# Performance work log

Hardware: AMD Instinct MI355X
Metric: run time of the kernel (lower is better)

Reference implementation:

```python
import jax, jax.numpy as jnp
import numpy as np

B = 32        # num graphs
N = 512       # nodes per graph (equal-sized blocks)
HID = 512     # hidden_dim
H = 8         # num_heads
E = 262144    # num edges
ED = 16       # edge feature dim


def setup_inputs() -> dict:
    key = jax.random.key(0)
    ks = jax.random.split(key, 12)
    x = jax.random.normal(ks[0], (B * N, HID), jnp.float32)
    # contiguous, sorted graph assignment (equal-sized graphs)
    batch = jnp.repeat(jnp.arange(B, dtype=jnp.int64), N)
    # within-graph random edges
    g = jax.random.randint(ks[1], (E,), 0, B)
    src = g * N + jax.random.randint(ks[2], (E,), 0, N)
    dst = g * N + jax.random.randint(ks[3], (E,), 0, N)
    edge_index = jnp.stack([src, dst]).astype(jnp.int64)
    edge_attr = jax.random.normal(ks[4], (E, ED), jnp.float32)
    s = 1.0 / np.sqrt(HID).astype(np.float32)
    Wq = jax.random.normal(ks[5], (HID, HID), jnp.float32) * s
    Wk = jax.random.normal(ks[6], (HID, HID), jnp.float32) * s
    Wv = jax.random.normal(ks[7], (HID, HID), jnp.float32) * s
    Wo = jax.random.normal(ks[8], (HID, HID), jnp.float32) * s
    We = jax.random.normal(ks[9], (ED, H), jnp.float32) * (1.0 / np.sqrt(ED).astype(np.float32))
    bq = jnp.zeros((HID,), jnp.float32)
    bk = jnp.zeros((HID,), jnp.float32)
    bv = jnp.zeros((HID,), jnp.float32)
    bo = jnp.zeros((HID,), jnp.float32)
    be = jnp.zeros((H,), jnp.float32)
    return dict(x=x, batch=batch, edge_index=edge_index, edge_attr=edge_attr,
                Wq=Wq, bq=bq, Wk=Wk, bk=bk, Wv=Wv, bv=bv, Wo=Wo, bo=bo,
                We=We, be=be, num_graphs=B)


def reference(x, batch, edge_index, edge_attr, Wq, bq, Wk, bk, Wv, bv, Wo, bo, We, be, num_graphs):
    n_total, hid = x.shape
    n = n_total // num_graphs           # nodes per graph (equal blocks)
    hd = hid // H                       # head_dim
    scale = 1.0 / jnp.sqrt(jnp.asarray(hd, x.dtype))
    q = (x @ Wq + bq).reshape(num_graphs, n, H, hd)
    k = (x @ Wk + bk).reshape(num_graphs, n, H, hd)
    v = (x @ Wv + bv).reshape(num_graphs, n, H, hd)
    # per-graph dense scores: [B, n(query), m(key), H]
    attn = jnp.einsum('bnhd,bmhd->bnmh', q, k) * scale
    # edge-bias scatter-add (edges are intra-graph; local coords via div/mod)
    eb = edge_attr @ We + be                      # [E, H]
    b_idx = edge_index[0] // n
    loc_src = edge_index[0] % n
    loc_dst = edge_index[1] % n
    attn = attn.at[b_idx, loc_src, loc_dst].add(eb)
    # softmax over key axis (torch dim=1 of 'nmh' == axis 2 here)
    attn = jax.nn.softmax(attn, axis=2)
    out = jnp.einsum('bnmh,bmhd->bnhd', attn, v).reshape(n_total, hid)
    return out @ Wo + bo
```

## Files before the change

### kernel.cpp

```cpp
#include <hip/hip_runtime.h>
#include <stdint.h>

typedef unsigned short u16;
typedef __bf16 bf16x8 __attribute__((ext_vector_type(8)));
typedef short  short8 __attribute__((ext_vector_type(8)));
typedef float  f32x4  __attribute__((ext_vector_type(4)));
typedef float  float4v __attribute__((ext_vector_type(4)));
typedef uint32_t u32x2 __attribute__((ext_vector_type(2)));

#define NG    32
#define NPG   512
#define HIDD  512
#define NH    8
#define HD    64
#define NE    262144
#define NNODE (NG*NPG)

__device__ __forceinline__ float fexp2(float x) { return __builtin_amdgcn_exp2f(x); }

__device__ __forceinline__ u16 f2bf(float f) {
  union { float f; uint32_t u; } x; x.f = f;
  uint32_t r = x.u + 0x7FFFu + ((x.u >> 16) & 1u);
  return (u16)(r >> 16);
}
__device__ __forceinline__ float bf2f(u16 b) {
  union { uint32_t u; float f; } x; x.u = ((uint32_t)b) << 16;
  return x.f;
}
__device__ __forceinline__ uint32_t pkbf(float a, float b) {
  __bf16 x = (__bf16)a, y = (__bf16)b;
  return (uint32_t)__builtin_bit_cast(u16, x) | ((uint32_t)__builtin_bit_cast(u16, y) << 16);
}
__device__ __forceinline__ bf16x8 ldfrag(const u16* p) {
  short8 t = *(const short8*)p;
  return __builtin_bit_cast(bf16x8, t);
}
__device__ __forceinline__ f32x4 mfma16(bf16x8 a, bf16x8 b, f32x4 c) {
  return __builtin_amdgcn_mfma_f32_16x16x32_bf16(a, b, c, 0, 0, 0);
}
__device__ __forceinline__ void gl2lds16(const void* g, void* l) {
  __builtin_amdgcn_global_load_lds((const __attribute__((address_space(1))) void*)g,
                                   (__attribute__((address_space(3))) void*)l, 16, 0, 0);
}
__device__ __forceinline__ void st(u16* p, float v)   { *p = f2bf(v); }
__device__ __forceinline__ void st(float* p, float v) { *p = v; }


__global__ void k_cast_x(const float* __restrict__ x, u16* __restrict__ xb) {
  size_t i = ((size_t)blockIdx.x * 256 + threadIdx.x) * 8;
  float4v v0 = *(const float4v*)(x + i);
  float4v v1 = *(const float4v*)(x + i + 4);
  short8 r;
  r[0]=(short)f2bf(v0[0]); r[1]=(short)f2bf(v0[1]); r[2]=(short)f2bf(v0[2]); r[3]=(short)f2bf(v0[3]);
  r[4]=(short)f2bf(v1[0]); r[5]=(short)f2bf(v1[1]); r[6]=(short)f2bf(v1[2]); r[7]=(short)f2bf(v1[3]);
  *(short8*)(xb + i) = r;
}

__global__ void k_transw(const float* __restrict__ W0, const float* __restrict__ W1,
                         const float* __restrict__ W2, const float* __restrict__ W3,
                         u16* __restrict__ wt) {
  const float* W = blockIdx.z==0 ? W0 : blockIdx.z==1 ? W1 : blockIdx.z==2 ? W2 : W3;
  u16* out = wt + (size_t)blockIdx.z * HIDD * HIDD;
  __shared__ float tl[32][33];
  int tx = threadIdx.x, ty = threadIdx.y;
  int x0 = blockIdx.x * 32, y0 = blockIdx.y * 32;
  #pragma unroll
  for (int i = 0; i < 4; ++i) tl[ty + i*8][tx] = W[(size_t)(y0 + ty + i*8) * HIDD + x0 + tx];
  __syncthreads();
  #pragma unroll
  for (int i = 0; i < 4; ++i) out[(size_t)(x0 + ty + i*8) * HIDD + (y0 + tx)] = f2bf(tl[tx][ty + i*8]);
}

__global__ void k_count2(const int* __restrict__ ei, int* __restrict__ counts) {
  int e = blockIdx.x * 256 + threadIdx.x;
  int src = ei[e];
  int dl  = ei[NE + e] & (NPG - 1);
  atomicAdd(&counts[src * 8 + (dl >> 6)], 1);
}

__global__ void k_scan_a(const int* __restrict__ counts, int* __restrict__ rowstart,
                         int* __restrict__ bsum) {
  __shared__ int arr[256];
  int t = threadIdx.x;
  int i = blockIdx.x * 256 + t;
  int c = counts[i];
  arr[t] = c;
  __syncthreads();
  for (int off = 1; off < 256; off <<= 1) {
    int v = (t >= off) ? arr[t - off] : 0;
    __syncthreads();
    arr[t] += v;
    __syncthreads();
  }
  rowstart[i] = arr[t] - c;
  if (t == 255) bsum[blockIdx.x] = arr[255];
}
__global__ void k_scan_b(int* __restrict__ bsum) {
  __shared__ int arr[512];
  int t = threadIdx.x;
  int c = bsum[t];
  arr[t] = c;
  __syncthreads();
  for (int off = 1; off < 512; off <<= 1) {
    int v = (t >= off) ? arr[t - off] : 0;
    __syncthreads();
    arr[t] += v;
    __syncthreads();
  }
  bsum[t] = arr[t] - c;
}
__global__ void k_scan_c(const int* __restrict__ bsum, int* __restrict__ rowstart) {
  int i = blockIdx.x * 256 + threadIdx.x;
  rowstart[i] += bsum[blockIdx.x];
  if (i == 0) rowstart[131072] = NE;
}

__global__ void k_fill(const int* __restrict__ ei, const float* __restrict__ ea,
                       const float* __restrict__ We, const float* __restrict__ be,
                       const int* __restrict__ rowstart, int* __restrict__ cursor,
                       uint32_t* __restrict__ packed) {
  __shared__ float w[128];
  __shared__ float bb[8];
  int t = threadIdx.x;
  if (t < 128) w[t] = We[t];
  if (t < 8)   bb[t] = be[t];
  __syncthreads();
  int e = blockIdx.x * 256 + t;
  int src = ei[e];
  int dl  = ei[NE + e] & (NPG - 1);
  const float* ap = ea + (size_t)e * 16;
  float a[16];
  #pragma unroll
  for (int i = 0; i < 16; i += 4) {
    float4v v = *(const float4v*)(ap + i);
    a[i]=v[0]; a[i+1]=v[1]; a[i+2]=v[2]; a[i+3]=v[3];
  }
  float acc[8];
  #pragma unroll
  for (int hh = 0; hh < 8; ++hh) acc[hh] = bb[hh];
  #pragma unroll
  for (int d = 0; d < 16; ++d)
    #pragma unroll
    for (int hh = 0; hh < 8; ++hh) acc[hh] += a[d] * w[d*8 + hh];
  int bin = src * 8 + (dl >> 6);
  int pos = atomicAdd(&cursor[bin], 1);
  size_t base = ((size_t)(rowstart[bin] + pos)) * 8;
  #pragma unroll
  for (int hh = 0; hh < 8; ++hh) {
    float m = fexp2(acc[hh] * 1.44269504089f);
    union { _Float16 hf; u16 us; } cv; cv.hf = (_Float16)m;
    packed[base + hh] = (uint32_t)(dl & 63) | ((uint32_t)cv.us << 16);
  }
}


template <typename OT, bool VOUT>
__device__ void gemm_body(u16* smem, const u16* __restrict__ A, const u16* __restrict__ Bt,
                          const float* __restrict__ bias, OT* __restrict__ C,
                          u16* __restrict__ vtg) {
  const int tid = threadIdx.x;
  const int w = tid >> 6, l = tid & 63, lr = l & 15, lg = l >> 4;
  const int bm0 = blockIdx.y * 128, bn0 = blockIdx.x * 128;
  const int wr = w >> 1, wc = w & 1;
  f32x4 acc[4][4];
  #pragma unroll
  for (int i = 0; i < 4; ++i)
    #pragma unroll
    for (int j = 0; j < 4; ++j) acc[i][j] = (f32x4){0.f, 0.f, 0.f, 0.f};

  const int o1 = w * 1024 + l * 16;
  auto stageAB = [&](int kt, int buf) {
    #pragma unroll
    for (int rnd = 0; rnd < 2; ++rnd) {
      const int o = rnd * 4096 + o1;
      const int row = o >> 6, colb = o & 63;
      gl2lds16((const char*)A  + ((size_t)(bm0 + row) * HIDD + kt * 32) * 2 + colb,
               (char*)smem + buf * 8192 + o);
      gl2lds16((const char*)Bt + ((size_t)(bn0 + row) * HIDD + kt * 32) * 2 + colb,
               (char*)smem + 16384 + buf * 8192 + o);
    }
  };

  stageAB(0, 0);
  for (int kt = 0; kt < 16; ++kt) {
    if (kt < 15) {
      stageAB(kt + 1, (kt + 1) & 1);
      asm volatile("s_waitcnt vmcnt(4)" ::: "memory");
    } else {
      asm volatile("s_waitcnt vmcnt(0)" ::: "memory");
    }
    __syncthreads();
    const u16* Ab = smem + (kt & 1) * 4096;
    const u16* Bb = smem + 8192 + (kt & 1) * 4096;
    bf16x8 af[4], bfr[4];
    #pragma unroll
    for (int i = 0; i < 4; ++i) af[i]  = ldfrag(&Ab[(wr*64 + i*16 + lr) * 32 + lg*8]);
    #pragma unroll
    for (int j = 0; j < 4; ++j) bfr[j] = ldfrag(&Bb[(wc*64 + j*16 + lr) * 32 + lg*8]);
    #pragma unroll
    for (int i = 0; i < 4; ++i)
      #pragma unroll
      for (int j = 0; j < 4; ++j)
        acc[i][j] = mfma16(af[i], bfr[j], acc[i][j]);
    __syncthreads();
  }

  if constexpr (VOUT) {
    #pragma unroll
    for (int j = 0; j < 4; ++j) {
      const int d = j * 16 + lr;
      const float bv = bias[bn0 + wc*64 + j*16 + lr];
      #pragma unroll
      for (int i = 0; i < 4; ++i) {
        const int t4 = wc * 2 + wr;
        const int byteo = t4 * 8192 + d * 128 + ((i*32 + lg*8) ^ ((d & 7) << 4));
        uint32_t lo = pkbf(acc[i][j][0] + bv, acc[i][j][1] + bv);
        uint32_t hi = pkbf(acc[i][j][2] + bv, acc[i][j][3] + bv);
        *(u32x2*)((char*)smem + byteo) = (u32x2){lo, hi};
      }
    }
    __syncthreads();
    const int b = bm0 >> 9, kt0 = (bm0 & 511) >> 6, h0 = bn0 >> 6;
    #pragma unroll
    for (int t4 = 0; t4 < 4; ++t4) {
      size_t base = ((size_t)(b * 8 + h0 + (t4 >> 1)) * 8 + kt0 + (t4 & 1)) * 4096;
      #pragma unroll
      for (int rnd = 0; rnd < 2; ++rnd) {
        int idx = rnd * 256 + tid;
        *(short8*)(vtg + base + idx * 8) = *(const short8*)&smem[t4 * 4096 + idx * 8];
      }
    }
  } else {
    #pragma unroll
    for (int j = 0; j < 4; ++j) {
      const int col = bn0 + wc*64 + j*16 + lr;
      const float bv = bias[col];
      #pragma unroll
      for (int i = 0; i < 4; ++i) {
        const int row0 = bm0 + wr*64 + i*16 + lg*4;
        #pragma unroll
        for (int q = 0; q < 4; ++q)
          st(&C[(size_t)(row0 + q) * HIDD + col], acc[i][j][q] + bv);
      }
    }
  }
}

__global__ __launch_bounds__(256, 3) void k_gemm_qkv(
    const u16* __restrict__ A, const u16* __restrict__ Wt,
    const float* __restrict__ b0, const float* __restrict__ b1, const float* __restrict__ b2,
    u16* __restrict__ O0, u16* __restrict__ O1, u16* __restrict__ vtg) {
  __shared__ u16 smem[16384];
  int z = blockIdx.z;
  const u16* Bt = Wt + (size_t)z * HIDD * HIDD;
  if (z == 0)      gemm_body<u16, false>(smem, A, Bt, b0, O0, nullptr);
  else if (z == 1) gemm_body<u16, false>(smem, A, Bt, b1, O1, nullptr);
  else             gemm_body<u16, true >(smem, A, Bt, b2, nullptr, vtg);
}

__global__ __launch_bounds__(256, 3) void k_gemm_out(
    const u16* __restrict__ A, const u16* __restrict__ Bt,
    const float* __restrict__ bias, float* __restrict__ C) {
  __shared__ u16 smem[16384];
  gemm_body<float, false>(smem, A, Bt, bias, C, nullptr);
}


__global__ __launch_bounds__(256, 4) void k_attn(
    const u16* __restrict__ qb, const u16* __restrict__ kb, const u16* __restrict__ vtg,
    const uint32_t* __restrict__ packed, const int* __restrict__ rowstart2,
    u16* __restrict__ ab) {
  __shared__ u16 kl[2][4096];
  __shared__ u16 vl[2][4096];
  __shared__ u16 pl[4][1024];
  const int tid = threadIdx.x, w = tid >> 6, l = tid & 63, lr = l & 15, lg = l >> 4;

  const int id = blockIdx.x;
  const int nid = (id & 7) * 256 + (id >> 3);
  const int q0 = (nid & 7) * 64;
  const int h  = (nid >> 3) & 7;
  const int b  = nid >> 6;
  const int bh = b * 8 + h;
  const int row = w * 16 + lr;
  const int grow = b * NPG + q0 + row;
  u16* plw = &pl[w][0];
  const int pswz = (lr & 7) << 4;

  bf16x8 qf[2];
  {
    const u16* qp = qb + (size_t)grow * HIDD + h * HD + lg * 8;
    qf[0] = ldfrag(qp);
    qf[1] = ldfrag(qp + 32);
  }

  auto stageK = [&](int kt, int buf) {
    #pragma unroll
    for (int rnd = 0; rnd < 2; ++rnd) {
      int o = rnd * 4096 + w * 1024 + l * 16;
      int key = o >> 7, db = o & 127;
      int col = db ^ ((key & 7) << 4);
      gl2lds16((const char*)kb + ((size_t)(b * NPG + kt * 64 + key) * HIDD + h * HD) * 2 + col,
               (char*)kl + buf * 8192 + o);
    }
  };
  auto stageV = [&](int kt, int buf) {
    #pragma unroll
    for (int rnd = 0; rnd < 2; ++rnd) {
      int o = rnd * 4096 + w * 1024 + l * 16;
      gl2lds16((const char*)vtg + ((size_t)(bh * 8 + kt)) * 8192 + o,
               (char*)vl + buf * 8192 + o);
    }
  };

  const float c1 = 0.125f * 1.44269504089f;
  float m2 = -1e30f;
  float rowsum = 0.f;
  f32x4 oacc[4];
  #pragma unroll
  for (int dt = 0; dt < 4; ++dt) oacc[dt] = (f32x4){0.f, 0.f, 0.f, 0.f};

  stageK(0, 0); stageV(0, 0); stageK(1, 1); stageV(1, 1);

  int eA = rowstart2[grow * 8];
  int eB = rowstart2[grow * 8 + 1];

  for (int kt = 0; kt < 8; ++kt) {
    int eC = (kt < 7) ? rowstart2[grow * 8 + kt + 2] : 0;
    if (kt < 7) asm volatile("s_waitcnt vmcnt(4)" ::: "memory");
    else        asm volatile("s_waitcnt vmcnt(0)" ::: "memory");
    __syncthreads();

    const u16* kB = kl[kt & 1];
    f32x4 s4[4];
    __builtin_amdgcn_s_setprio(1);
    #pragma unroll
    for (int sub = 0; sub < 4; ++sub) {
      s4[sub] = (f32x4){0.f, 0.f, 0.f, 0.f};
      int key = sub * 16 + lr;
      #pragma unroll
      for (int ks = 0; ks < 2; ++ks) {
        int db = ((ks * 32 + lg * 8) * 2) ^ ((key & 7) << 4);
        bf16x8 kf = ldfrag(&kB[(key * 128 + db) >> 1]);
        s4[sub] = mfma16(kf, qf[ks], s4[sub]);
      }
    }
    __builtin_amdgcn_s_setprio(0);

    float tm = s4[0][0];
    #pragma unroll
    for (int sub = 0; sub < 4; ++sub)
      #pragma unroll
      for (int e = 0; e < 4; ++e) tm = fmaxf(tm, s4[sub][e]);
    tm = fmaxf(tm, __shfl_xor(tm, 16, 64));
    tm = fmaxf(tm, __shfl_xor(tm, 32, 64));
    float tmc = tm * c1;
    if (__any(tmc > m2 + 8.0f)) {
      float m2n = fmaxf(m2, tmc);
      float rsc = fexp2(m2 - m2n);
      m2 = m2n;
      rowsum *= rsc;
      #pragma unroll
      for (int dt = 0; dt < 4; ++dt) oacc[dt] *= rsc;
    }

    #pragma unroll
    for (int sub = 0; sub < 4; ++sub) {
      float p0 = fexp2(__builtin_fmaf(s4[sub][0], c1, -m2));
      float p1 = fexp2(__builtin_fmaf(s4[sub][1], c1, -m2));
      float p2 = fexp2(__builtin_fmaf(s4[sub][2], c1, -m2));
      float p3 = fexp2(__builtin_fmaf(s4[sub][3], c1, -m2));
      rowsum += (p0 + p1) + (p2 + p3);
      uint32_t lo = pkbf(p0, p1);
      uint32_t hi = pkbf(p2, p3);
      *(u32x2*)((char*)plw + lr * 128 + ((sub * 32 + lg * 8) ^ pswz)) = (u32x2){lo, hi};
    }
    asm volatile("s_waitcnt lgkmcnt(0)" ::: "memory");
    __builtin_amdgcn_sched_barrier(0);

    {
      float delta = 0.f;
      for (int s = eA; s < eB; ++s) {
        uint32_t u = packed[(size_t)s * 8 + h];
        int dl = (int)(u & 63u);
        if ((dl & 3) == lg) {
          union { u16 us; _Float16 hf; } cv; cv.us = (u16)(u >> 16);
          float mult = (float)cv.hf;
          int idx = (lr * 128 + ((dl * 2) ^ pswz)) >> 1;
          float old = bf2f(plw[idx]);
          u16 nb = f2bf(old * mult);
          plw[idx] = nb;
          delta += bf2f(nb) - old;
        }
      }
      rowsum += delta;
    }
    asm volatile("s_waitcnt lgkmcnt(0)" ::: "memory");
    __builtin_amdgcn_sched_barrier(0);

    const u16* vB = vl[kt & 1];
    __builtin_amdgcn_s_setprio(1);
    #pragma unroll
    for (int ks = 0; ks < 2; ++ks) {
      bf16x8 pa = ldfrag(&plw[(lr * 128 + ((ks * 64 + lg * 16) ^ pswz)) >> 1]);
      #pragma unroll
      for (int dt = 0; dt < 4; ++dt) {
        int d = dt * 16 + lr;
        bf16x8 vf = ldfrag(&vB[(d * 128 + ((ks * 64 + lg * 16) ^ ((d & 7) << 4))) >> 1]);
        oacc[dt] = mfma16(vf, pa, oacc[dt]);
      }
    }
    __builtin_amdgcn_s_setprio(0);

    __syncthreads();
    if (kt < 6) { stageK(kt + 2, kt & 1); stageV(kt + 2, kt & 1); }
    eA = eB; eB = eC;
  }

  float tot = rowsum + __shfl_xor(rowsum, 16, 64);
  tot += __shfl_xor(tot, 32, 64);
  float inv = 1.0f / tot;
  #pragma unroll
  for (int dt = 0; dt < 4; ++dt) {
    uint32_t lo = pkbf(oacc[dt][0] * inv, oacc[dt][1] * inv);
    uint32_t hi = pkbf(oacc[dt][2] * inv, oacc[dt][3] * inv);
    *(u32x2*)(ab + (size_t)grow * HIDD + h * HD + dt * 16 + lg * 4) = (u32x2){lo, hi};
  }
}


extern "C" void kernel_launch(void* const* d_in, const int* in_sizes, int n_in,
                              void* d_out, int out_size, void* d_ws, size_t ws_size,
                              hipStream_t stream) {
  const float* x  = (const float*)d_in[0];
  const int*   ei = (const int*)d_in[2];
  const float* ea = (const float*)d_in[3];
  const float* Wq = (const float*)d_in[4];  const float* bq = (const float*)d_in[5];
  const float* Wk = (const float*)d_in[6];  const float* bk = (const float*)d_in[7];
  const float* Wv = (const float*)d_in[8];  const float* bv = (const float*)d_in[9];
  const float* Wo = (const float*)d_in[10]; const float* bo = (const float*)d_in[11];
  const float* We = (const float*)d_in[12]; const float* be = (const float*)d_in[13];

  char* ws = (char*)d_ws;
  const size_t MB = 1 << 20;
  u16*  xb  = (u16*)(ws);
  u16*  wt  = (u16*)(ws + 16*MB);
  u16*  qbp = (u16*)(ws + 18*MB);
  u16*  kbp = (u16*)(ws + 34*MB);
  u16*  vtg = (u16*)(ws + 50*MB);
  uint32_t* packed = (uint32_t*)(ws + 66*MB);
  int*  rowstart2 = (int*)(ws + 74*MB);
  int*  bsum      = (int*)(ws + 74*MB + 640*1024);
  int*  counts2  = (int*)(ws + 50*MB);
  int*  cursor2  = (int*)(ws + 50*MB + 512*1024);
  u16*  ab = xb;

  (void)hipMemsetAsync(counts2, 0, 2 * 512 * 1024, stream);

  k_cast_x<<<dim3(NNODE * HIDD / (256 * 8)), 256, 0, stream>>>(x, xb);
  k_transw<<<dim3(16, 16, 4), dim3(32, 8, 1), 0, stream>>>(Wq, Wk, Wv, Wo, wt);
  k_count2<<<dim3(NE / 256), 256, 0, stream>>>(ei, counts2);
  k_scan_a<<<dim3(512), 256, 0, stream>>>(counts2, rowstart2, bsum);
  k_scan_b<<<dim3(1), 512, 0, stream>>>(bsum);
  k_scan_c<<<dim3(512), 256, 0, stream>>>(bsum, rowstart2);
  k_fill<<<dim3(NE / 256), 256, 0, stream>>>(ei, ea, We, be, rowstart2, cursor2, packed);

  k_gemm_qkv<<<dim3(HIDD / 128, NNODE / 128, 3), 256, 0, stream>>>(
      xb, wt, bq, bk, bv, qbp, kbp, vtg);

  k_attn<<<dim3(2048), 256, 0, stream>>>(qbp, kbp, vtg, packed, rowstart2, ab);

  k_gemm_out<<<dim3(HIDD / 128, NNODE / 128, 1), 256, 0, stream>>>(
      ab, wt + (size_t)3 * HIDD * HIDD, bo, (float*)d_out);
}
```

Measured before the change: 177.8 us.

## Single-buffer K/V LDS tiles to raise attention occupancy and prefetch edge records

Replaces the double-buffered K and V shared-memory tiles with single buffers, cutting LDS use per block so launch bounds can rise from 4 to 6 blocks per CU. Each tile is now loaded only after the previous one is consumed, so the loop waits on all outstanding loads every iteration and loses in-block overlap. In exchange it relies on more resident blocks to hide memory latency. It also software-pipelines the sparse edge-record loads by issuing the first record early and prefetching the next record inside the bias loop.

```diff
diff --git a/kernel.cpp b/kernel.cpp
--- a/kernel.cpp
+++ b/kernel.cpp
@@ -266,12 +266,12 @@
 }
 
 
-__global__ __launch_bounds__(256, 4) void k_attn(
+__global__ __launch_bounds__(256, 6) void k_attn(
     const u16* __restrict__ qb, const u16* __restrict__ kb, const u16* __restrict__ vtg,
     const uint32_t* __restrict__ packed, const int* __restrict__ rowstart2,
     u16* __restrict__ ab) {
-  __shared__ u16 kl[2][4096];
-  __shared__ u16 vl[2][4096];
+  __shared__ u16 kl[4096];
+  __shared__ u16 vl[4096];
   __shared__ u16 pl[4][1024];
   const int tid = threadIdx.x, w = tid >> 6, l = tid & 63, lr = l & 15, lg = l >> 4;
 
@@ -293,22 +293,22 @@
     qf[1] = ldfrag(qp + 32);
   }
 
-  auto stageK = [&](int kt, int buf) {
+  auto stageK = [&](int kt) {
     #pragma unroll
     for (int rnd = 0; rnd < 2; ++rnd) {
       int o = rnd * 4096 + w * 1024 + l * 16;
       int key = o >> 7, db = o & 127;
       int col = db ^ ((key & 7) << 4);
       gl2lds16((const char*)kb + ((size_t)(b * NPG + kt * 64 + key) * HIDD + h * HD) * 2 + col,
-               (char*)kl + buf * 8192 + o);
+               (char*)kl + o);
     }
   };
-  auto stageV = [&](int kt, int buf) {
+  auto stageV = [&](int kt) {
     #pragma unroll
     for (int rnd = 0; rnd < 2; ++rnd) {
       int o = rnd * 4096 + w * 1024 + l * 16;
       gl2lds16((const char*)vtg + ((size_t)(bh * 8 + kt)) * 8192 + o,
-               (char*)vl + buf * 8192 + o);
+               (char*)vl + o);
     }
   };
 
@@ -319,18 +319,19 @@
   #pragma unroll
   for (int dt = 0; dt < 4; ++dt) oacc[dt] = (f32x4){0.f, 0.f, 0.f, 0.f};
 
-  stageK(0, 0); stageV(0, 0); stageK(1, 1); stageV(1, 1);
+  stageK(0); stageV(0);
 
   int eA = rowstart2[grow * 8];
   int eB = rowstart2[grow * 8 + 1];
 
   for (int kt = 0; kt < 8; ++kt) {
+    asm volatile("s_waitcnt vmcnt(0)" ::: "memory");
+    __syncthreads();
+
     int eC = (kt < 7) ? rowstart2[grow * 8 + kt + 2] : 0;
-    if (kt < 7) asm volatile("s_waitcnt vmcnt(4)" ::: "memory");
-    else        asm volatile("s_waitcnt vmcnt(0)" ::: "memory");
-    __syncthreads();
-
-    const u16* kB = kl[kt & 1];
+    int s0c = (eA < eB) ? eA : 0;
+    uint32_t u0 = packed[(size_t)s0c * 8 + h];
+
     f32x4 s4[4];
     __builtin_amdgcn_s_setprio(1);
     #pragma unroll
@@ -340,7 +341,7 @@
       #pragma unroll
       for (int ks = 0; ks < 2; ++ks) {
         int db = ((ks * 32 + lg * 8) * 2) ^ ((key & 7) << 4);
-        bf16x8 kf = ldfrag(&kB[(key * 128 + db) >> 1]);
+        bf16x8 kf = ldfrag(&kl[(key * 128 + db) >> 1]);
         s4[sub] = mfma16(kf, qf[ks], s4[sub]);
       }
     }
@@ -379,11 +380,13 @@
 
     {
       float delta = 0.f;
+      uint32_t u = u0;
       for (int s = eA; s < eB; ++s) {
-        uint32_t u = packed[(size_t)s * 8 + h];
-        int dl = (int)(u & 63u);
+        uint32_t ucur = u;
+        if (s + 1 < eB) u = packed[(size_t)(s + 1) * 8 + h];
+        int dl = (int)(ucur & 63u);
         if ((dl & 3) == lg) {
-          union { u16 us; _Float16 hf; } cv; cv.us = (u16)(u >> 16);
+          union { u16 us; _Float16 hf; } cv; cv.us = (u16)(ucur >> 16);
           float mult = (float)cv.hf;
           int idx = (lr * 128 + ((dl * 2) ^ pswz)) >> 1;
           float old = bf2f(plw[idx]);
@@ -397,7 +400,6 @@
     asm volatile("s_waitcnt lgkmcnt(0)" ::: "memory");
     __builtin_amdgcn_sched_barrier(0);
 
-    const u16* vB = vl[kt & 1];
     __builtin_amdgcn_s_setprio(1);
     #pragma unroll
     for (int ks = 0; ks < 2; ++ks) {
@@ -405,14 +407,14 @@
       #pragma unroll
       for (int dt = 0; dt < 4; ++dt) {
         int d = dt * 16 + lr;
-        bf16x8 vf = ldfrag(&vB[(d * 128 + ((ks * 64 + lg * 16) ^ ((d & 7) << 4))) >> 1]);
+        bf16x8 vf = ldfrag(&vl[(d * 128 + ((ks * 64 + lg * 16) ^ ((d & 7) << 4))) >> 1]);
         oacc[dt] = mfma16(vf, pa, oacc[dt]);
       }
     }
     __builtin_amdgcn_s_setprio(0);
 
     __syncthreads();
-    if (kt < 6) { stageK(kt + 2, kt & 1); stageV(kt + 2, kt & 1); }
+    if (kt < 7) { stageK(kt + 1); stageV(kt + 1); }
     eA = eB; eB = eC;
   }
 
```

Result: no change. 179.7 us (+1.1%).
